# Performance work log

Measured on AMD Instinct MI355X. Metric: run time of the kernel, lower is better.

Reference implementation:

```python
import jax, jax.numpy as jnp
import numpy as np

B, H, P, K, E, BN = 8, 256, 1024, 32, 4, 64


def setup_inputs() -> dict:
    key = jax.random.key(0)
    ks = jax.random.split(key, 8)
    current = jax.random.normal(ks[0], (B, H, P), dtype=jnp.float32)
    neighbor_features = jax.random.normal(ks[1], (B, H, P, K), dtype=jnp.float32)
    # binary {0,1} validity mask, stored as float like the torch module expects
    neighbor_validity = jax.random.randint(ks[2], (B, 1, P, K), 0, 2).astype(jnp.float32)
    edge_features = jax.random.normal(ks[3], (B, E, P, K), dtype=jnp.float32)
    # 1x1 Conv2d weights flattened to matrices: (out_ch, in_ch)
    w1 = jax.random.normal(ks[4], (BN, 2 * H + E), dtype=jnp.float32) * 0.05
    b1 = jnp.zeros((BN,), dtype=jnp.float32)
    w2 = jax.random.normal(ks[5], (BN,), dtype=jnp.float32) * 0.05  # second conv: out_ch=1
    b2 = jnp.zeros((), dtype=jnp.float32)
    return {
        "current": current,
        "neighbor_features": neighbor_features,
        "neighbor_validity": neighbor_validity,
        "edge_features": edge_features,
        "w1": w1,
        "b1": b1,
        "w2": w2,
        "b2": b2,
    }


def reference(current, neighbor_features, neighbor_validity, edge_features, w1, b1, w2, b2):
    h_dim = current.shape[1]
    # Split the 1x1-conv weight along the concat axis so we never materialize
    # the [B, 2H+E, P, K] concatenated tensor (same math as cat + conv1x1).
    w1c = w1[:, :h_dim]            # acts on broadcast center features
    w1n = w1[:, h_dim:2 * h_dim]   # acts on neighbor features
    w1e = w1[:, 2 * h_dim:]        # acts on edge features

    hid = (
        jnp.einsum("bcp,oc->bop", current, w1c)[:, :, :, None]
        + jnp.einsum("bcpk,oc->bopk", neighbor_features, w1n)
        + jnp.einsum("bcpk,oc->bopk", edge_features, w1e)
        + b1[None, :, None, None]
    )
    hid = jax.nn.relu(hid)                                  # (B, BN, P, K)
    logits = jnp.einsum("bopk,o->bpk", hid, w2) + b2        # (B, P, K)

    valid = neighbor_validity[:, 0] > 0.5                   # (B, P, K) bool
    logits = jnp.where(valid, logits, -jnp.inf)
    has_any = jnp.any(valid, axis=-1, keepdims=True)        # (B, P, 1)
    logits_safe = jnp.where(has_any, logits, 0.0)           # all-masked rows -> 0 logits
    weights = jax.nn.softmax(logits_safe, axis=-1)
    weights = jnp.where(has_any & valid, weights, 0.0)      # zero weight on pads / empty rows

    pooled = jnp.einsum("bcpk,bpk->bcp", neighbor_features, weights)
    return pooled
```

## Files before the change

kernel.cpp:

```cpp
#include <hip/hip_runtime.h>
#include <math.h>


#define B_ 8
#define H_ 256
#define P_ 1024
#define K_ 32
#define E_ 4
#define BN_ 64

typedef __attribute__((ext_vector_type(8))) short short8;
typedef __attribute__((ext_vector_type(4))) float floatx4;

__device__ __forceinline__ unsigned short bf16_rne(float f) {
  unsigned u = __float_as_uint(f);
  u += 0x7fffu + ((u >> 16) & 1u);
  return (unsigned short)(u >> 16);
}
__device__ __forceinline__ unsigned pack_bf16_rne(float lo, float hi) {
  unsigned u0 = __float_as_uint(lo);
  u0 += 0x7fffu + ((u0 >> 16) & 1u);
  unsigned u1 = __float_as_uint(hi);
  u1 += 0x7fffu + ((u1 >> 16) & 1u);
  return (u0 >> 16) | (u1 & 0xffff0000u);
}

__device__ __forceinline__ void async_cp4(const float* g, float* l) {
  __builtin_amdgcn_global_load_lds(
      (const __attribute__((address_space(1))) unsigned*)g,
      (__attribute__((address_space(3))) unsigned*)l, 4, 0, 0);
}

__global__ __launch_bounds__(256) void prep_kernel(
    const float* __restrict__ w1, unsigned short* __restrict__ w1m) {
  int i = blockIdx.x * 256 + threadIdx.x;
  if (i >= 4 * 17 * 64 * 8) return;
  int j = i & 7, lane = (i >> 3) & 63;
  int kt = i >> 9;
  int mt = kt / 17, ki = kt % 17;
  int o = mt * 16 + (lane & 15);
  int c = ki * 32 + (lane >> 4) * 8 + j;
  float v = (c < 516) ? w1[o * 516 + c] : 0.f;
  w1m[i] = bf16_rne(v);
}

__global__ __launch_bounds__(256, 2) void soft_attn_agg_kernel(
    const float* __restrict__ cur,
    const float* __restrict__ nf,
    const float* __restrict__ nv,
    const float* __restrict__ ef,
    const unsigned short* __restrict__ w1m,
    const float* __restrict__ b1,
    const float* __restrict__ w2,
    float* __restrict__ out) {
  __shared__ unsigned s_tile[128 * 132];
  __shared__ float s_raw[16 * 128];
  __shared__ unsigned short s_curb[4][264];
  __shared__ unsigned s_edge[4][32][2];
  __shared__ float s_valid[128];
  __shared__ float s_b1v[BN_];
  __shared__ float s_w2v[BN_];
  __shared__ float s_lg[128];
  __shared__ float s_wt[128];

  const int t = threadIdx.x;
  const unsigned bid = blockIdx.x;
  const unsigned xcd = bid & 7u, sx = bid >> 3;
  const int b = (int)(sx >> 5);
  const int pg = (int)(xcd * 32u + (sx & 31u));
  const int p0 = pg * 4;

  const int w = t >> 6;
  const int lane = t & 63;
  const int q = lane >> 4;
  const int ln15 = lane & 15;

  {
    const float* cb = cur + ((size_t)b * H_ + t) * P_ + p0;
    float4 ca = *(const float4*)cb;
    s_curb[0][t] = bf16_rne(ca.x);
    s_curb[1][t] = bf16_rne(ca.y);
    s_curb[2][t] = bf16_rne(ca.z);
    s_curb[3][t] = bf16_rne(ca.w);
  }
  if (t < 128) {
    s_valid[t] = nv[((size_t)b * P_ + p0) * K_ + t];
    const int pl = t >> 5, k = t & 31;
    const float* ep = ef + ((size_t)b * E_ * P_ + p0 + pl) * K_ + k;
    float e0 = ep[0];
    float e1 = ep[(size_t)(P_ * K_)];
    float e2 = ep[(size_t)(2 * P_ * K_)];
    float e3 = ep[(size_t)(3 * P_ * K_)];
    s_edge[pl][k][0] = pack_bf16_rne(e0, e1);
    s_edge[pl][k][1] = pack_bf16_rne(e2, e3);
  } else if (t < 192) {
    s_b1v[t - 128] = b1[t - 128];
  } else {
    s_w2v[t - 192] = w2[t - 192];
  }

  const float* nf_b = nf + ((size_t)b * H_ * P_ + p0) * K_;
  for (int ch = 0; ch < 16; ++ch) {
#pragma unroll
    for (int r = 0; r < 4; ++r) {
      const int cl = 4 * w + r;
      const float* g = nf_b + (size_t)(ch * 16 + cl) * (P_ * K_);
      float* l = &s_raw[cl * 128];
      async_cp4(g + lane, l);
      async_cp4(g + 64 + lane, l + 64);
    }
    __syncthreads();
#pragma unroll
    for (int j = 0; j < 2; ++j) {
      const int r0 = 4 * w + 2 * j;
      const int cp = ch * 8 + 2 * w + j;
#pragma unroll
      for (int i = 0; i < 2; ++i) {
        const int n = lane + 64 * i;
        float fe = s_raw[r0 * 128 + n];
        float fo = s_raw[(r0 + 1) * 128 + n];
        s_tile[n * 132 + cp] = pack_bf16_rne(fe, fo);
      }
    }
  }
  __syncthreads();

  floatx4 acc[4][2];
#pragma unroll
  for (int mt = 0; mt < 4; ++mt) {
    floatx4 binit = *(const floatx4*)&s_b1v[mt * 16 + q * 4];
    acc[mt][0] = binit;
    acc[mt][1] = binit;
  }
  const unsigned short* w1m_l = w1m + (size_t)lane * 8;

#pragma unroll
  for (int ki = 0; ki < 8; ++ki) {
    short8 bc = *(const short8*)&s_curb[w][ki * 32 + q * 8];
#pragma unroll
    for (int mt = 0; mt < 4; ++mt) {
      short8 a = *(const short8*)(w1m_l + (size_t)(mt * 17 + ki) * 512);
      acc[mt][0] = __builtin_amdgcn_mfma_f32_16x16x32_bf16(a, bc, acc[mt][0], 0, 0, 0);
      acc[mt][1] = __builtin_amdgcn_mfma_f32_16x16x32_bf16(a, bc, acc[mt][1], 0, 0, 0);
    }
  }
#pragma unroll
  for (int ck = 0; ck < 8; ++ck) {
    short8 bn0 = *(const short8*)(s_tile + (32 * w + ln15) * 132 + 16 * ck + 4 * q);
    short8 bn1 = *(const short8*)(s_tile + (32 * w + 16 + ln15) * 132 + 16 * ck + 4 * q);
#pragma unroll
    for (int mt = 0; mt < 4; ++mt) {
      short8 a = *(const short8*)(w1m_l + (size_t)(mt * 17 + 8 + ck) * 512);
      acc[mt][0] = __builtin_amdgcn_mfma_f32_16x16x32_bf16(a, bn0, acc[mt][0], 0, 0, 0);
      acc[mt][1] = __builtin_amdgcn_mfma_f32_16x16x32_bf16(a, bn1, acc[mt][1], 0, 0, 0);
    }
  }
  {
    union { unsigned u[4]; short8 s; } ub0, ub1;
    *(uint2*)&ub0.u[0] = *(const uint2*)&s_edge[w][ln15][0];
    ub0.u[2] = 0u; ub0.u[3] = 0u;
    *(uint2*)&ub1.u[0] = *(const uint2*)&s_edge[w][16 + ln15][0];
    ub1.u[2] = 0u; ub1.u[3] = 0u;
#pragma unroll
    for (int mt = 0; mt < 4; ++mt) {
      short8 a = *(const short8*)(w1m_l + (size_t)(mt * 17 + 16) * 512);
      acc[mt][0] = __builtin_amdgcn_mfma_f32_16x16x32_bf16(a, ub0.s, acc[mt][0], 0, 0, 0);
      acc[mt][1] = __builtin_amdgcn_mfma_f32_16x16x32_bf16(a, ub1.s, acc[mt][1], 0, 0, 0);
    }
  }

#pragma unroll
  for (int nti = 0; nti < 2; ++nti) {
    float lp = 0.f;
#pragma unroll
    for (int mt = 0; mt < 4; ++mt) {
      const floatx4 w2v = *(const floatx4*)&s_w2v[mt * 16 + q * 4];
#pragma unroll
      for (int r = 0; r < 4; ++r)
        lp = fmaf(fmaxf(acc[mt][nti][r], 0.f), w2v[r], lp);
    }
    lp += __shfl_xor(lp, 16);
    lp += __shfl_xor(lp, 32);
    if (lane < 16) s_lg[(2 * w + nti) * 16 + ln15] = lp;
  }
  __syncthreads();

  if (t < 128) {
    float lg = s_lg[t];
    bool v = s_valid[t] > 0.5f;
    float ml = v ? lg : -INFINITY;
#pragma unroll
    for (int m = 1; m < 32; m <<= 1) ml = fmaxf(ml, __shfl_xor(ml, m));
    float e = v ? __expf(lg - ml) : 0.f;
    float ssum = e;
#pragma unroll
    for (int m = 1; m < 32; m <<= 1) ssum += __shfl_xor(ssum, m);
    s_wt[t] = (ml > -INFINITY) ? (e / ssum) : 0.f;
  }
  __syncthreads();

  {
    const int cpr = t & 127, ph = t >> 7;
    const int nb = ph * 64;
    float a0e = 0.f, a0o = 0.f, a1e = 0.f, a1o = 0.f;
#pragma unroll
    for (int k = 0; k < K_; ++k) {
      const unsigned u0 = s_tile[(nb + k) * 132 + cpr];
      const unsigned u1 = s_tile[(nb + 32 + k) * 132 + cpr];
      const float wt0 = s_wt[nb + k];
      const float wt1 = s_wt[nb + 32 + k];
      a0e = fmaf(__uint_as_float(u0 << 16), wt0, a0e);
      a0o = fmaf(__uint_as_float(u0 & 0xffff0000u), wt0, a0o);
      a1e = fmaf(__uint_as_float(u1 << 16), wt1, a1e);
      a1o = fmaf(__uint_as_float(u1 & 0xffff0000u), wt1, a1o);
    }
    float* op = out + ((size_t)b * H_ + 2 * cpr) * P_ + p0 + 2 * ph;
    float2 ve; ve.x = a0e; ve.y = a1e;
    float2 vo; vo.x = a0o; vo.y = a1o;
    *(float2*)op = ve;
    *(float2*)(op + P_) = vo;
  }
}

extern "C" void kernel_launch(void* const* d_in, const int* in_sizes, int n_in,
                              void* d_out, int out_size, void* d_ws,
                              size_t ws_size, hipStream_t stream) {
  const float* cur = (const float*)d_in[0];
  const float* nf  = (const float*)d_in[1];
  const float* nv  = (const float*)d_in[2];
  const float* ef  = (const float*)d_in[3];
  const float* w1  = (const float*)d_in[4];
  const float* b1  = (const float*)d_in[5];
  const float* w2  = (const float*)d_in[6];

  unsigned short* w1m = (unsigned short*)d_ws;
  prep_kernel<<<(4 * 17 * 64 * 8 + 255) / 256, 256, 0, stream>>>(w1, w1m);
  soft_attn_agg_kernel<<<B_ * P_ / 4, 256, 0, stream>>>(
      cur, nf, nv, ef, w1m, b1, w2, (float*)d_out);
}
```

Baseline: 400.3 us.

## Triple-buffer neighbor-feature DMA, swizzle LDS tile, drop weight prep kernel

The neighbor-feature staging loop changes from one __syncthreads-separated chunk at a time to a triple-buffered 16-byte global_load_lds pipeline driven by explicit vmcnt waits, so loads overlap the bf16 packing. The LDS tile drops its padding and uses an XOR swizzle to avoid bank conflicts. The separate w1 prep kernel is removed: each block reads fp32 w1 and converts it in-register with v_cvt_pk_bf16_f32, which saves a launch but adds redundant global loads and conversions per block. Validity is kept in a register, and the logit and weight buffers reuse the raw staging space to cut shared memory.

```diff
diff --git a/kernel.cpp b/kernel.cpp
--- a/kernel.cpp
+++ b/kernel.cpp
@@ -17,51 +17,42 @@
   u += 0x7fffu + ((u >> 16) & 1u);
   return (unsigned short)(u >> 16);
 }
-__device__ __forceinline__ unsigned pack_bf16_rne(float lo, float hi) {
-  unsigned u0 = __float_as_uint(lo);
-  u0 += 0x7fffu + ((u0 >> 16) & 1u);
-  unsigned u1 = __float_as_uint(hi);
-  u1 += 0x7fffu + ((u1 >> 16) & 1u);
-  return (u0 >> 16) | (u1 & 0xffff0000u);
-}
-
-__device__ __forceinline__ void async_cp4(const float* g, float* l) {
+__device__ __forceinline__ unsigned pack_bf16(float lo, float hi) {
+  unsigned r;
+  asm("v_cvt_pk_bf16_f32 %0, %1, %2" : "=v"(r) : "v"(lo), "v"(hi));
+  return r;
+}
+
+__device__ __forceinline__ void async_cp16(const float* g, float* l) {
   __builtin_amdgcn_global_load_lds(
       (const __attribute__((address_space(1))) unsigned*)g,
-      (__attribute__((address_space(3))) unsigned*)l, 4, 0, 0);
-}
-
-__global__ __launch_bounds__(256) void prep_kernel(
-    const float* __restrict__ w1, unsigned short* __restrict__ w1m) {
-  int i = blockIdx.x * 256 + threadIdx.x;
-  if (i >= 4 * 17 * 64 * 8) return;
-  int j = i & 7, lane = (i >> 3) & 63;
-  int kt = i >> 9;
-  int mt = kt / 17, ki = kt % 17;
-  int o = mt * 16 + (lane & 15);
-  int c = ki * 32 + (lane >> 4) * 8 + j;
-  float v = (c < 516) ? w1[o * 516 + c] : 0.f;
-  w1m[i] = bf16_rne(v);
-}
+      (__attribute__((address_space(3))) unsigned*)l, 16, 0, 0);
+}
+
+__device__ __forceinline__ unsigned* tile_ptr(unsigned* tile, int n, int cp) {
+  return tile + n * 128 + ((((cp >> 2) ^ (n & 7)) << 2) | (cp & 3));
+}
+
+#define STR_(x) #x
+#define VMWAIT(n) asm volatile("s_waitcnt vmcnt(" STR_(n) ")")
 
 __global__ __launch_bounds__(256, 2) void soft_attn_agg_kernel(
     const float* __restrict__ cur,
     const float* __restrict__ nf,
     const float* __restrict__ nv,
     const float* __restrict__ ef,
-    const unsigned short* __restrict__ w1m,
+    const float* __restrict__ w1,
     const float* __restrict__ b1,
     const float* __restrict__ w2,
     float* __restrict__ out) {
-  __shared__ unsigned s_tile[128 * 132];
-  __shared__ float s_raw[16 * 128];
+  __shared__ unsigned s_tile[128 * 128];
+  __shared__ float s_raw[3 * 8 * 128];
   __shared__ unsigned short s_curb[4][264];
   __shared__ unsigned s_edge[4][32][2];
-  __shared__ float s_valid[128];
   __shared__ float s_b1v[BN_];
   __shared__ float s_w2v[BN_];
-  __shared__ float s_lg[128];
-  __shared__ float s_wt[128];
+  float* const s_lg = s_raw;
+  float* const s_wt = s_raw + 128;
 
   const int t = threadIdx.x;
   const unsigned bid = blockIdx.x;
@@ -74,6 +65,21 @@
   const int lane = t & 63;
   const int q = lane >> 4;
   const int ln15 = lane & 15;
+
+  const float* nf_b = nf + ((size_t)b * H_ * P_ + p0) * K_;
+
+#define ISSUE_DMA(ch, bufbase)                                               \
+  async_cp16(nf_b + (size_t)((ch)*8 + 2 * w + (lane >> 5)) * (P_ * K_) +     \
+                 ((lane & 31) << 2),                                         \
+             (bufbase) + 2 * w * 128)
+
+  float* const rbuf0 = s_raw;
+  float* const rbuf1 = s_raw + 1024;
+  float* const rbuf2 = s_raw + 2048;
+
+  ISSUE_DMA(0, rbuf0);
+  ISSUE_DMA(1, rbuf1);
+  ISSUE_DMA(2, rbuf2);
 
   {
     const float* cb = cur + ((size_t)b * H_ + t) * P_ + p0;
@@ -83,46 +89,47 @@
     s_curb[2][t] = bf16_rne(ca.z);
     s_curb[3][t] = bf16_rne(ca.w);
   }
+  float my_valid = 0.f;
   if (t < 128) {
-    s_valid[t] = nv[((size_t)b * P_ + p0) * K_ + t];
+    my_valid = nv[((size_t)b * P_ + p0) * K_ + t];
     const int pl = t >> 5, k = t & 31;
     const float* ep = ef + ((size_t)b * E_ * P_ + p0 + pl) * K_ + k;
     float e0 = ep[0];
     float e1 = ep[(size_t)(P_ * K_)];
     float e2 = ep[(size_t)(2 * P_ * K_)];
     float e3 = ep[(size_t)(3 * P_ * K_)];
-    s_edge[pl][k][0] = pack_bf16_rne(e0, e1);
-    s_edge[pl][k][1] = pack_bf16_rne(e2, e3);
+    s_edge[pl][k][0] = pack_bf16(e0, e1);
+    s_edge[pl][k][1] = pack_bf16(e2, e3);
   } else if (t < 192) {
     s_b1v[t - 128] = b1[t - 128];
   } else {
     s_w2v[t - 192] = w2[t - 192];
   }
 
-  const float* nf_b = nf + ((size_t)b * H_ * P_ + p0) * K_;
-  for (int ch = 0; ch < 16; ++ch) {
-#pragma unroll
-    for (int r = 0; r < 4; ++r) {
-      const int cl = 4 * w + r;
-      const float* g = nf_b + (size_t)(ch * 16 + cl) * (P_ * K_);
-      float* l = &s_raw[cl * 128];
-      async_cp4(g + lane, l);
-      async_cp4(g + 64 + lane, l + 64);
-    }
-    __syncthreads();
-#pragma unroll
-    for (int j = 0; j < 2; ++j) {
-      const int r0 = 4 * w + 2 * j;
-      const int cp = ch * 8 + 2 * w + j;
-#pragma unroll
-      for (int i = 0; i < 2; ++i) {
-        const int n = lane + 64 * i;
-        float fe = s_raw[r0 * 128 + n];
-        float fo = s_raw[(r0 + 1) * 128 + n];
-        s_tile[n * 132 + cp] = pack_bf16_rne(fe, fo);
-      }
-    }
-  }
+#define PIPE_ITER(ch, bufbase, VMN, DO_ISSUE)                                \
+  {                                                                          \
+    VMWAIT(VMN);                                                             \
+    __builtin_amdgcn_sched_barrier(0);                                       \
+    const float* rb0 = (bufbase) + 2 * w * 128;                              \
+    const float* rb1 = rb0 + 128;                                            \
+    float fe0 = rb0[lane], fo0 = rb1[lane];                                  \
+    float fe1 = rb0[lane + 64], fo1 = rb1[lane + 64];                        \
+    unsigned pk0 = pack_bf16(fe0, fo0);                                      \
+    unsigned pk1 = pack_bf16(fe1, fo1);                                      \
+    __builtin_amdgcn_sched_barrier(0);                                       \
+    if (DO_ISSUE) ISSUE_DMA((ch) + 3, bufbase);                              \
+    const int cpv = 4 * (ch) + w;                                            \
+    *tile_ptr(s_tile, lane, cpv) = pk0;                                      \
+    *tile_ptr(s_tile, lane + 64, cpv) = pk1;                                 \
+  }
+
+  for (int c3 = 0; c3 < 30; c3 += 3) {
+    PIPE_ITER(c3, rbuf0, 2, (c3) < 29);
+    PIPE_ITER(c3 + 1, rbuf1, 2, (c3 + 1) < 29);
+    PIPE_ITER(c3 + 2, rbuf2, 2, (c3 + 2) < 29);
+  }
+  PIPE_ITER(30, rbuf0, 1, false);
+  PIPE_ITER(31, rbuf1, 0, false);
   __syncthreads();
 
   floatx4 acc[4][2];
@@ -132,27 +139,41 @@
     acc[mt][0] = binit;
     acc[mt][1] = binit;
   }
-  const unsigned short* w1m_l = w1m + (size_t)lane * 8;
+  const float* w1base = w1 + (size_t)ln15 * 516 + q * 8;
 
 #pragma unroll
   for (int ki = 0; ki < 8; ++ki) {
     short8 bc = *(const short8*)&s_curb[w][ki * 32 + q * 8];
 #pragma unroll
     for (int mt = 0; mt < 4; ++mt) {
-      short8 a = *(const short8*)(w1m_l + (size_t)(mt * 17 + ki) * 512);
-      acc[mt][0] = __builtin_amdgcn_mfma_f32_16x16x32_bf16(a, bc, acc[mt][0], 0, 0, 0);
-      acc[mt][1] = __builtin_amdgcn_mfma_f32_16x16x32_bf16(a, bc, acc[mt][1], 0, 0, 0);
+      const float* ap = w1base + (size_t)mt * (16 * 516) + ki * 32;
+      float4 f0 = *(const float4*)ap;
+      float4 f1 = *(const float4*)(ap + 4);
+      union { unsigned u[4]; short8 s; } a;
+      a.u[0] = pack_bf16(f0.x, f0.y);
+      a.u[1] = pack_bf16(f0.z, f0.w);
+      a.u[2] = pack_bf16(f1.x, f1.y);
+      a.u[3] = pack_bf16(f1.z, f1.w);
+      acc[mt][0] = __builtin_amdgcn_mfma_f32_16x16x32_bf16(a.s, bc, acc[mt][0], 0, 0, 0);
+      acc[mt][1] = __builtin_amdgcn_mfma_f32_16x16x32_bf16(a.s, bc, acc[mt][1], 0, 0, 0);
     }
   }
 #pragma unroll
   for (int ck = 0; ck < 8; ++ck) {
-    short8 bn0 = *(const short8*)(s_tile + (32 * w + ln15) * 132 + 16 * ck + 4 * q);
-    short8 bn1 = *(const short8*)(s_tile + (32 * w + 16 + ln15) * 132 + 16 * ck + 4 * q);
-#pragma unroll
-    for (int mt = 0; mt < 4; ++mt) {
-      short8 a = *(const short8*)(w1m_l + (size_t)(mt * 17 + 8 + ck) * 512);
-      acc[mt][0] = __builtin_amdgcn_mfma_f32_16x16x32_bf16(a, bn0, acc[mt][0], 0, 0, 0);
-      acc[mt][1] = __builtin_amdgcn_mfma_f32_16x16x32_bf16(a, bn1, acc[mt][1], 0, 0, 0);
+    short8 bn0 = *(const short8*)tile_ptr(s_tile, 32 * w + ln15, (4 * ck + q) << 2);
+    short8 bn1 = *(const short8*)tile_ptr(s_tile, 32 * w + 16 + ln15, (4 * ck + q) << 2);
+#pragma unroll
+    for (int mt = 0; mt < 4; ++mt) {
+      const float* ap = w1base + (size_t)mt * (16 * 516) + 256 + ck * 32;
+      float4 f0 = *(const float4*)ap;
+      float4 f1 = *(const float4*)(ap + 4);
+      union { unsigned u[4]; short8 s; } a;
+      a.u[0] = pack_bf16(f0.x, f0.y);
+      a.u[1] = pack_bf16(f0.z, f0.w);
+      a.u[2] = pack_bf16(f1.x, f1.y);
+      a.u[3] = pack_bf16(f1.z, f1.w);
+      acc[mt][0] = __builtin_amdgcn_mfma_f32_16x16x32_bf16(a.s, bn0, acc[mt][0], 0, 0, 0);
+      acc[mt][1] = __builtin_amdgcn_mfma_f32_16x16x32_bf16(a.s, bn1, acc[mt][1], 0, 0, 0);
     }
   }
   {
@@ -163,9 +184,18 @@
     ub1.u[2] = 0u; ub1.u[3] = 0u;
 #pragma unroll
     for (int mt = 0; mt < 4; ++mt) {
-      short8 a = *(const short8*)(w1m_l + (size_t)(mt * 17 + 16) * 512);
-      acc[mt][0] = __builtin_amdgcn_mfma_f32_16x16x32_bf16(a, ub0.s, acc[mt][0], 0, 0, 0);
-      acc[mt][1] = __builtin_amdgcn_mfma_f32_16x16x32_bf16(a, ub1.s, acc[mt][1], 0, 0, 0);
+      union { unsigned u[4]; short8 s; } ae;
+      if (q == 0) {
+        const float* ap = w1 + (size_t)(mt * 16 + ln15) * 516 + 512;
+        float4 f0 = *(const float4*)ap;
+        ae.u[0] = pack_bf16(f0.x, f0.y);
+        ae.u[1] = pack_bf16(f0.z, f0.w);
+      } else {
+        ae.u[0] = 0u; ae.u[1] = 0u;
+      }
+      ae.u[2] = 0u; ae.u[3] = 0u;
+      acc[mt][0] = __builtin_amdgcn_mfma_f32_16x16x32_bf16(ae.s, ub0.s, acc[mt][0], 0, 0, 0);
+      acc[mt][1] = __builtin_amdgcn_mfma_f32_16x16x32_bf16(ae.s, ub1.s, acc[mt][1], 0, 0, 0);
     }
   }
 
@@ -187,7 +217,7 @@
 
   if (t < 128) {
     float lg = s_lg[t];
-    bool v = s_valid[t] > 0.5f;
+    bool v = my_valid > 0.5f;
     float ml = v ? lg : -INFINITY;
 #pragma unroll
     for (int m = 1; m < 32; m <<= 1) ml = fmaxf(ml, __shfl_xor(ml, m));
@@ -205,8 +235,8 @@
     float a0e = 0.f, a0o = 0.f, a1e = 0.f, a1o = 0.f;
 #pragma unroll
     for (int k = 0; k < K_; ++k) {
-      const unsigned u0 = s_tile[(nb + k) * 132 + cpr];
-      const unsigned u1 = s_tile[(nb + 32 + k) * 132 + cpr];
+      const unsigned u0 = *tile_ptr(s_tile, nb + k, cpr);
+      const unsigned u1 = *tile_ptr(s_tile, nb + 32 + k, cpr);
       const float wt0 = s_wt[nb + k];
       const float wt1 = s_wt[nb + 32 + k];
       a0e = fmaf(__uint_as_float(u0 << 16), wt0, a0e);
@@ -232,9 +262,8 @@
   const float* w1  = (const float*)d_in[4];
   const float* b1  = (const float*)d_in[5];
   const float* w2  = (const float*)d_in[6];
-
-  unsigned short* w1m = (unsigned short*)d_ws;
-  prep_kernel<<<(4 * 17 * 64 * 8 + 255) / 256, 256, 0, stream>>>(w1, w1m);
+  (void)d_ws; (void)ws_size;
+
   soft_attn_agg_kernel<<<B_ * P_ / 4, 256, 0, stream>>>(
-      cur, nf, nv, ef, w1m, b1, w2, (float*)d_out);
-}
+      cur, nf, nv, ef, w1, b1, w2, (float*)d_out);
+}
```

New measurement: 432.2 us. +8.0%, slower.
